# Performance work log

Measured on AMD Instinct MI355X. Metric: run time of the kernel, lower is better.

## Reference

```python
import jax, jax.numpy as jnp
import numpy as np

B, T, D, H, L = 512, 1024, 2, 32, 16  # batch, seq_len, input_dim, hidden_dim, latent_dim


def lstm_layer(x, W_ih, W_hh, b_ih, b_hh):
    """Single torch-semantics LSTM layer. x: [B, T, D_in] -> (h_seq [B,T,H], c_final [B,H]).
    Gate order matches torch: i, f, g, o."""
    Bb = x.shape[0]
    Hh = W_hh.shape[1]
    # Precompute input projection for all timesteps (one big GEMM).
    xW = jnp.einsum('btd,gd->btg', x, W_ih) + (b_ih + b_hh)  # [B, T, 4H]

    def step(carry, xw_t):
        h, c = carry
        gates = xw_t + h @ W_hh.T  # [B, 4H]
        i, f, g, o = jnp.split(gates, 4, axis=-1)
        i = jax.nn.sigmoid(i)
        f = jax.nn.sigmoid(f)
        g = jnp.tanh(g)
        o = jax.nn.sigmoid(o)
        c = f * c + i * g
        h = o * jnp.tanh(c)
        return (h, c), h

    h0 = jnp.zeros((Bb, Hh), x.dtype)
    c0 = jnp.zeros((Bb, Hh), x.dtype)
    (_, cT), h_seq = jax.lax.scan(step, (h0, c0), jnp.swapaxes(xW, 0, 1))
    return jnp.swapaxes(h_seq, 0, 1), cT


def setup_inputs() -> dict:
    key = jax.random.key(0)
    ks = jax.random.split(key, 20)
    s = 1.0 / np.sqrt(H)  # torch LSTM/Linear init scale
    u = lambda k, shape: jax.random.uniform(k, shape, jnp.float32, -s, s)
    inp = {"x": jax.random.normal(ks[0], (B, T, D), jnp.float32)}
    dims_in = [D, H, H]
    for l in range(3):
        inp[f"W_ih{l}"] = u(ks[1 + 4 * l], (4 * H, dims_in[l]))
        inp[f"W_hh{l}"] = u(ks[2 + 4 * l], (4 * H, H))
        inp[f"b_ih{l}"] = u(ks[3 + 4 * l], (4 * H,))
        inp[f"b_hh{l}"] = u(ks[4 + 4 * l], (4 * H,))
    inp["W_mean"] = u(ks[13], (L, H))
    inp["b_mean"] = u(ks[14], (L,))
    inp["W_logvar"] = u(ks[15], (L, H))
    inp["b_logvar"] = u(ks[16], (L,))
    return inp


def reference(x, W_ih0, W_hh0, b_ih0, b_hh0, W_ih1, W_hh1, b_ih1, b_hh1,
              W_ih2, W_hh2, b_ih2, b_hh2, W_mean, b_mean, W_logvar, b_logvar):
    # 3-layer LSTM (dropout inactive at inference); only top-layer final cell is used.
    h, _ = lstm_layer(x, W_ih0, W_hh0, b_ih0, b_hh0)
    h, _ = lstm_layer(h, W_ih1, W_hh1, b_ih1, b_hh1)
    _, c3 = lstm_layer(h, W_ih2, W_hh2, b_ih2, b_hh2)  # c3: [B, H]
    mean = c3 @ W_mean.T + b_mean        # [B, L]
    log_var = c3 @ W_logvar.T + b_logvar  # [B, L]
    return (mean, log_var)
```

## Files before the change

kernel.cpp:

```cpp
#include <hip/hip_runtime.h>

#define T_LEN 1024
#define HID   32
#define LDIM  16
#define BATCH 512
#define NB    8
#define NT    768
#define ROWB  80
#define SLOTB (8 * ROWB)
#define SLOT_ALL (4 * SLOTB)
#define NSLOT 8
#define LOG2E 1.44269504f

typedef _Float16 half8  __attribute__((ext_vector_type(8)));
typedef _Float16 half2v __attribute__((ext_vector_type(2)));
typedef float    f32x4  __attribute__((ext_vector_type(4)));
typedef unsigned u32;
typedef unsigned u32x4  __attribute__((ext_vector_type(4)));

#if defined(__has_builtin)
#if __has_builtin(__builtin_amdgcn_rcpf)
#define FAST_RCP(x) __builtin_amdgcn_rcpf(x)
#endif
#if __has_builtin(__builtin_amdgcn_exp2f)
#define FAST_EXP2(x) __builtin_amdgcn_exp2f(x)
#endif
#endif
#ifndef FAST_RCP
#define FAST_RCP(x) (1.0f / (x))
#endif
#ifndef FAST_EXP2
#define FAST_EXP2(x) __expf(0.69314718f * (x))
#endif

#define MFMA(a, b, c) __builtin_amdgcn_mfma_f32_16x16x32_f16((a), (b), (c), 0, 0, 0)

__device__ __forceinline__ void waitc(const u32* p, u32 need) {
    while (__hip_atomic_load(p, __ATOMIC_ACQUIRE, __HIP_MEMORY_SCOPE_WORKGROUP) < need)
        __builtin_amdgcn_s_sleep(1);
}

__global__ __launch_bounds__(NT, 1)
void lstm_encoder_kernel(const float* __restrict__ x,
                         const float* __restrict__ Wih0, const float* __restrict__ Whh0,
                         const float* __restrict__ bih0, const float* __restrict__ bhh0,
                         const float* __restrict__ Wih1, const float* __restrict__ Whh1,
                         const float* __restrict__ bih1, const float* __restrict__ bhh1,
                         const float* __restrict__ Wih2, const float* __restrict__ Whh2,
                         const float* __restrict__ bih2, const float* __restrict__ bhh2,
                         const float* __restrict__ Wm,  const float* __restrict__ bm,
                         const float* __restrict__ Wlv, const float* __restrict__ blv,
                         float* __restrict__ out)
{
    const int b0   = blockIdx.x * NB;
    const int tid  = threadIdx.x;
    const int lane = tid & 63;
    const int wave = tid >> 6;
    const int l    = wave >> 2;
    const int w    = wave & 3;
    const int n    = lane & 15;
    const int kc   = lane >> 4;
    const int nb   = n & 7;
    const int hi   = n >> 3;
    const int unit = 8 * w + 2 * kc + hi;

    __shared__ u32 xs[T_LEN * NB];
    __shared__ __align__(16) unsigned char ring[NSLOT * SLOT_ALL];
    __shared__ u32 cnt[48];
    __shared__ float cbuf[NB * HID];

    for (int i = tid; i < NB * T_LEN; i += NT) {
        const int nn = i >> 10, t = i & (T_LEN - 1);
        const float2 v = *(const float2*)(x + ((size_t)(b0 + nn) * T_LEN + t) * 2);
        half2v p; p[0] = (_Float16)v.x; p[1] = (_Float16)v.y;
        xs[t * NB + nn] = __builtin_bit_cast(u32, p);
    }
    for (int i = tid; i < (int)(sizeof(ring) / 4); i += NT) ((u32*)ring)[i] = 0u;
    if (tid < 48) cnt[tid] = 0u;

    const float* Wih = (l == 0) ? Wih0 : (l == 1) ? Wih1 : Wih2;
    const float* Whh = (l == 0) ? Whh0 : (l == 1) ? Whh1 : Whh2;
    const float* bih = (l == 0) ? bih0 : (l == 1) ? bih1 : bih2;
    const float* bhh = (l == 0) ? bhh0 : (l == 1) ? bhh1 : bhh2;

    half8 aprev[2], aself[2];
    f32x4 biasC[2];
#pragma unroll
    for (int tau = 0; tau < 2; ++tau) {
        const int   rho  = n & 1, uloc = n >> 1;
        const int   base = (tau == 0) ? (rho ? 32 : 0) : (rho ? 96 : 64);
        const int   R    = base + 8 * w + uloc;
        const float sc   = (tau == 1 && rho == 0) ? (2.0f * LOG2E) : LOG2E;
#pragma unroll
        for (int i2 = 0; i2 < 8; ++i2) {
            const int kk = kc * 8 + i2;
            aself[tau][i2] = (_Float16)(Whh[R * HID + kk] * sc);
            aprev[tau][i2] = (_Float16)(((l == 0) ? ((kk < 2) ? Wih[R * 2 + kk] : 0.0f)
                                                  : Wih[R * HID + kk]) * sc);
        }
#pragma unroll
        for (int r = 0; r < 4; ++r) {
            const int   rr    = r & 1, uD = 2 * kc + (r >> 1);
            const int   baseD = (tau == 0) ? (rr ? 32 : 0) : (rr ? 96 : 64);
            const int   RD    = baseD + 8 * w + uD;
            const float scD   = (tau == 1 && rr == 0) ? (2.0f * LOG2E) : LOG2E;
            biasC[tau][r] = (bih[RD] + bhh[RD]) * scD;
        }
    }

    const int off_r0 = ((l == 0) ? 3 : (l - 1)) * SLOTB + nb * ROWB + kc * 16;
    const int off_r1 = l * SLOTB + nb * ROWB + kc * 16;
    const int off_w  = l * SLOTB + nb * ROWB + unit * 2;
    const int off_x  = 3 * SLOTB + lane * ROWB;
    const bool xf    = (wave == 0) && (lane < NB);

    u32* cs = &cnt[l * 16];
    u32* cp = &cnt[((l > 0) ? (l - 1) : 0) * 16];
    u32* cn = &cnt[((l < 2) ? (l + 1) : 0) * 16];

    float cc = 0.0f;

    __syncthreads();
    if (xf) *(u32*)(ring + off_x) = xs[lane];
    __syncthreads();

    for (int tb = 0; tb < T_LEN; tb += NSLOT) {
#pragma unroll
        for (int s = 0; s < NSLOT; ++s) {
            const int t = tb + s;
            if (t > 0)                 waitc(cs, 4u * (u32)t);
            if (l > 0)                 waitc(cp, 4u * (u32)(t + 1));
            if (l < 2 && t >= NSLOT)   waitc(cn, 4u * (u32)(t - 7));

            u32 xw = 0;
            if (xf) {
                const int tn = (t + 1 < T_LEN) ? (t + 1) : (T_LEN - 1);
                xw = xs[tn * NB + lane];
            }
            const half8 bf0 = __builtin_bit_cast(half8,
                *(const u32x4*)(ring + s * SLOT_ALL + off_r0));
            const half8 bf1 = __builtin_bit_cast(half8,
                *(const u32x4*)(ring + ((s + 7) & 7) * SLOT_ALL + off_r1));

            f32x4 ac0 = MFMA(aprev[0], bf0, biasC[0]);
            f32x4 ac1 = MFMA(aprev[1], bf0, biasC[1]);
            ac0 = MFMA(aself[0], bf1, ac0);
            ac1 = MFMA(aself[1], bf1, ac1);

            const float ai  = hi ? ac0[2] : ac0[0];
            const float af_ = hi ? ac0[3] : ac0[1];
            const float ag  = hi ? ac1[2] : ac1[0];
            const float ao  = hi ? ac1[3] : ac1[1];

            const float ei = FAST_EXP2(-ai);
            const float ef = FAST_EXP2(-af_);
            const float eg = FAST_EXP2(-ag);
            const float eo = FAST_EXP2(-ao);
            const float p1  = (1.0f + ei) * (1.0f + eg);
            const float den = p1 * (1.0f + ef);
            const float tmn = (1.0f - eg) * (1.0f + ef);
            float c_ = fmaf(cc, p1, tmn) * FAST_RCP(den);
            c_ = fminf(fmaxf(c_, -20.0f), 20.0f);
            cc = c_;
            const float ec = FAST_EXP2(-2.0f * LOG2E * c_);
            const float hv = (1.0f - ec) * FAST_RCP((1.0f + eo) * (1.0f + ec));

            *(_Float16*)(ring + s * SLOT_ALL + off_w) = (_Float16)hv;
            if (xf) *(u32*)(ring + ((s + 1) & 7) * SLOT_ALL + off_x) = xw;

            if (lane == 0)
                __hip_atomic_fetch_add(cs, 1u, __ATOMIC_RELEASE,
                                       __HIP_MEMORY_SCOPE_WORKGROUP);
        }
    }

    if (l == 2) cbuf[nb * HID + unit] = cc;
    __syncthreads();

    if (tid < NB * 2 * LDIM) {
        const int  nn = tid >> 5;
        const int  o  = tid & 31;
        const bool is_mean = (o < LDIM);
        const int  jo = o & (LDIM - 1);
        const float* W  = is_mean ? Wm : Wlv;
        float acc = is_mean ? bm[jo] : blv[jo];
#pragma unroll
        for (int k = 0; k < HID; ++k) acc = fmaf(W[jo * HID + k], cbuf[nn * HID + k], acc);
        out[(is_mean ? 0 : (size_t)BATCH * LDIM) + (size_t)(b0 + nn) * LDIM + jo] = acc;
    }
}

extern "C" void kernel_launch(void* const* d_in, const int* in_sizes, int n_in,
                              void* d_out, int out_size, void* d_ws, size_t ws_size,
                              hipStream_t stream) {
    const float* x    = (const float*)d_in[0];
    const float* Wih0 = (const float*)d_in[1];
    const float* Whh0 = (const float*)d_in[2];
    const float* bih0 = (const float*)d_in[3];
    const float* bhh0 = (const float*)d_in[4];
    const float* Wih1 = (const float*)d_in[5];
    const float* Whh1 = (const float*)d_in[6];
    const float* bih1 = (const float*)d_in[7];
    const float* bhh1 = (const float*)d_in[8];
    const float* Wih2 = (const float*)d_in[9];
    const float* Whh2 = (const float*)d_in[10];
    const float* bih2 = (const float*)d_in[11];
    const float* bhh2 = (const float*)d_in[12];
    const float* Wm   = (const float*)d_in[13];
    const float* bm   = (const float*)d_in[14];
    const float* Wlv  = (const float*)d_in[15];
    const float* blv  = (const float*)d_in[16];
    float* out = (float*)d_out;

    lstm_encoder_kernel<<<dim3(BATCH / NB), dim3(NT), 0, stream>>>(
        x, Wih0, Whh0, bih0, bhh0, Wih1, Whh1, bih1, bhh1,
        Wih2, Whh2, bih2, bhh2, Wm, bm, Wlv, blv, out);
}
```

Before: 437.9 us.

## Halve batch per block to 4, 2 waves per layer with 4 MFMAs each

Drops the batch per block from 8 to 4 and the threads from 768 to 384, so each layer runs on 2 waves instead of 4. Each wave now issues 4 MFMAs per input, sharing one B fragment across 16 hidden units. Layer 0 no longer runs an input MFMA; it adds the 2-wide input projection with scalar FMAs from the xs array, which also removes the x-slot ring traffic. The change also reorders waves across layers, raises wave priority around the critical compute, and lengthens the spin sleep. Twice as many blocks (128) gives more CU parallelism, at the cost of a longer serial chain of MFMAs per wave per timestep.

```diff
diff --git a/kernel.cpp b/kernel.cpp
--- a/kernel.cpp
+++ b/kernel.cpp
@@ -4,11 +4,8 @@
 #define HID   32
 #define LDIM  16
 #define BATCH 512
-#define NB    8
-#define NT    768
-#define ROWB  80
-#define SLOTB (8 * ROWB)
-#define SLOT_ALL (4 * SLOTB)
+#define NB    4
+#define NT    384
 #define NSLOT 8
 #define LOG2E 1.44269504f
 
@@ -37,7 +34,7 @@
 
 __device__ __forceinline__ void waitc(const u32* p, u32 need) {
     while (__hip_atomic_load(p, __ATOMIC_ACQUIRE, __HIP_MEMORY_SCOPE_WORKGROUP) < need)
-        __builtin_amdgcn_s_sleep(1);
+        __builtin_amdgcn_s_sleep(2);
 }
 
 __global__ __launch_bounds__(NT, 1)
@@ -56,23 +53,23 @@
     const int tid  = threadIdx.x;
     const int lane = tid & 63;
     const int wave = tid >> 6;
-    const int l    = wave >> 2;
-    const int w    = wave & 3;
+    const int l    = (wave < 2) ? 1 : (wave < 4) ? 0 : 2;
+    const int v    = wave & 1;
     const int n    = lane & 15;
     const int kc   = lane >> 4;
-    const int nb   = n & 7;
-    const int hi   = n >> 3;
-    const int unit = 8 * w + 2 * kc + hi;
+    const int nb   = n & 3;
+    const int hi   = n >> 2;
+    const int unit = 16 * v + 4 * hi + kc;
 
     __shared__ u32 xs[T_LEN * NB];
-    __shared__ __align__(16) unsigned char ring[NSLOT * SLOT_ALL];
+    __shared__ __align__(16) u32x4 ring[3][NSLOT][4][NB];
     __shared__ u32 cnt[48];
     __shared__ float cbuf[NB * HID];
 
     for (int i = tid; i < NB * T_LEN; i += NT) {
         const int nn = i >> 10, t = i & (T_LEN - 1);
-        const float2 v = *(const float2*)(x + ((size_t)(b0 + nn) * T_LEN + t) * 2);
-        half2v p; p[0] = (_Float16)v.x; p[1] = (_Float16)v.y;
+        const float2 vv = *(const float2*)(x + ((size_t)(b0 + nn) * T_LEN + t) * 2);
+        half2v p; p[0] = (_Float16)vv.x; p[1] = (_Float16)vv.y;
         xs[t * NB + nn] = __builtin_bit_cast(u32, p);
     }
     for (int i = tid; i < (int)(sizeof(ring) / 4); i += NT) ((u32*)ring)[i] = 0u;
@@ -83,36 +80,33 @@
     const float* bih = (l == 0) ? bih0 : (l == 1) ? bih1 : bih2;
     const float* bhh = (l == 0) ? bhh0 : (l == 1) ? bhh1 : bhh2;
 
-    half8 aprev[2], aself[2];
-    f32x4 biasC[2];
-#pragma unroll
-    for (int tau = 0; tau < 2; ++tau) {
-        const int   rho  = n & 1, uloc = n >> 1;
-        const int   base = (tau == 0) ? (rho ? 32 : 0) : (rho ? 96 : 64);
-        const int   R    = base + 8 * w + uloc;
-        const float sc   = (tau == 1 && rho == 0) ? (2.0f * LOG2E) : LOG2E;
-#pragma unroll
-        for (int i2 = 0; i2 < 8; ++i2) {
-            const int kk = kc * 8 + i2;
-            aself[tau][i2] = (_Float16)(Whh[R * HID + kk] * sc);
-            aprev[tau][i2] = (_Float16)(((l == 0) ? ((kk < 2) ? Wih[R * 2 + kk] : 0.0f)
-                                                  : Wih[R * HID + kk]) * sc);
+    half8 aprev[4], aself[4];
+    f32x4 biasC[4];
+    float wx0v[4], wx1v[4];
+#pragma unroll
+    for (int tau = 0; tau < 4; ++tau) {
+        const int   R  = (n & 3) * 32 + 16 * v + 4 * tau + (n >> 2);
+        const float sc = ((n & 3) == 2) ? (2.0f * LOG2E) : LOG2E;
+#pragma unroll
+        for (int e = 0; e < 8; ++e) {
+            const int kk = 8 * kc + e;
+            aself[tau][e] = (_Float16)(Whh[R * HID + kk] * sc);
+            aprev[tau][e] = (l > 0) ? (_Float16)(Wih[R * HID + kk] * sc) : (_Float16)0.0f;
         }
 #pragma unroll
         for (int r = 0; r < 4; ++r) {
-            const int   rr    = r & 1, uD = 2 * kc + (r >> 1);
-            const int   baseD = (tau == 0) ? (rr ? 32 : 0) : (rr ? 96 : 64);
-            const int   RD    = baseD + 8 * w + uD;
-            const float scD   = (tau == 1 && rr == 0) ? (2.0f * LOG2E) : LOG2E;
+            const int   RD  = r * 32 + 16 * v + 4 * tau + kc;
+            const float scD = (r == 2) ? (2.0f * LOG2E) : LOG2E;
             biasC[tau][r] = (bih[RD] + bhh[RD]) * scD;
         }
     }
-
-    const int off_r0 = ((l == 0) ? 3 : (l - 1)) * SLOTB + nb * ROWB + kc * 16;
-    const int off_r1 = l * SLOTB + nb * ROWB + kc * 16;
-    const int off_w  = l * SLOTB + nb * ROWB + unit * 2;
-    const int off_x  = 3 * SLOTB + lane * ROWB;
-    const bool xf    = (wave == 0) && (lane < NB);
+#pragma unroll
+    for (int r = 0; r < 4; ++r) {
+        const int   RD  = r * 32 + unit;
+        const float scD = (r == 2) ? (2.0f * LOG2E) : LOG2E;
+        wx0v[r] = (l == 0) ? Wih[RD * 2 + 0] * scD : 0.0f;
+        wx1v[r] = (l == 0) ? Wih[RD * 2 + 1] * scD : 0.0f;
+    }
 
     u32* cs = &cnt[l * 16];
     u32* cp = &cnt[((l > 0) ? (l - 1) : 0) * 16];
@@ -121,41 +115,52 @@
     float cc = 0.0f;
 
     __syncthreads();
-    if (xf) *(u32*)(ring + off_x) = xs[lane];
-    __syncthreads();
 
     for (int tb = 0; tb < T_LEN; tb += NSLOT) {
 #pragma unroll
         for (int s = 0; s < NSLOT; ++s) {
             const int t = tb + s;
-            if (t > 0)                 waitc(cs, 4u * (u32)t);
-            if (l > 0)                 waitc(cp, 4u * (u32)(t + 1));
-            if (l < 2 && t >= NSLOT)   waitc(cn, 4u * (u32)(t - 7));
-
-            u32 xw = 0;
-            if (xf) {
-                const int tn = (t + 1 < T_LEN) ? (t + 1) : (T_LEN - 1);
-                xw = xs[tn * NB + lane];
+            if (t > 0)               waitc(cs, 2u * (u32)t);
+            if (l > 0)               waitc(cp, 2u * (u32)(t + 1));
+            if (l < 2 && t >= NSLOT) waitc(cn, 2u * (u32)(t - (NSLOT - 1)));
+
+            const u32x4 bf1 = ring[l][(s + NSLOT - 1) & (NSLOT - 1)][kc][nb];
+
+            __builtin_amdgcn_s_setprio(1);
+            f32x4 a0, a1, a2, a3;
+            if (l == 0) {
+                a0 = MFMA(aself[0], __builtin_bit_cast(half8, bf1), biasC[0]);
+                a1 = MFMA(aself[1], __builtin_bit_cast(half8, bf1), biasC[1]);
+                a2 = MFMA(aself[2], __builtin_bit_cast(half8, bf1), biasC[2]);
+                a3 = MFMA(aself[3], __builtin_bit_cast(half8, bf1), biasC[3]);
+            } else {
+                const u32x4 bf0 = ring[l - 1][s][kc][nb];
+                a0 = MFMA(aprev[0], __builtin_bit_cast(half8, bf0), biasC[0]);
+                a1 = MFMA(aprev[1], __builtin_bit_cast(half8, bf0), biasC[1]);
+                a2 = MFMA(aprev[2], __builtin_bit_cast(half8, bf0), biasC[2]);
+                a3 = MFMA(aprev[3], __builtin_bit_cast(half8, bf0), biasC[3]);
+                a0 = MFMA(aself[0], __builtin_bit_cast(half8, bf1), a0);
+                a1 = MFMA(aself[1], __builtin_bit_cast(half8, bf1), a1);
+                a2 = MFMA(aself[2], __builtin_bit_cast(half8, bf1), a2);
+                a3 = MFMA(aself[3], __builtin_bit_cast(half8, bf1), a3);
             }
-            const half8 bf0 = __builtin_bit_cast(half8,
-                *(const u32x4*)(ring + s * SLOT_ALL + off_r0));
-            const half8 bf1 = __builtin_bit_cast(half8,
-                *(const u32x4*)(ring + ((s + 7) & 7) * SLOT_ALL + off_r1));
-
-            f32x4 ac0 = MFMA(aprev[0], bf0, biasC[0]);
-            f32x4 ac1 = MFMA(aprev[1], bf0, biasC[1]);
-            ac0 = MFMA(aself[0], bf1, ac0);
-            ac1 = MFMA(aself[1], bf1, ac1);
-
-            const float ai  = hi ? ac0[2] : ac0[0];
-            const float af_ = hi ? ac0[3] : ac0[1];
-            const float ag  = hi ? ac1[2] : ac1[0];
-            const float ao  = hi ? ac1[3] : ac1[1];
-
-            const float ei = FAST_EXP2(-ai);
-            const float ef = FAST_EXP2(-af_);
-            const float eg = FAST_EXP2(-ag);
-            const float eo = FAST_EXP2(-ao);
+
+#define SELR(r) ((hi & 2) ? ((hi & 1) ? a3[r] : a2[r]) : ((hi & 1) ? a1[r] : a0[r]))
+            float gi = SELR(0), gf = SELR(1), gg = SELR(2), go = SELR(3);
+#undef SELR
+            if (l == 0) {
+                const half2v xp = __builtin_bit_cast(half2v, xs[t * NB + nb]);
+                const float x0 = (float)xp[0], x1 = (float)xp[1];
+                gi = fmaf(wx1v[0], x1, fmaf(wx0v[0], x0, gi));
+                gf = fmaf(wx1v[1], x1, fmaf(wx0v[1], x0, gf));
+                gg = fmaf(wx1v[2], x1, fmaf(wx0v[2], x0, gg));
+                go = fmaf(wx1v[3], x1, fmaf(wx0v[3], x0, go));
+            }
+
+            const float ei  = FAST_EXP2(-gi);
+            const float ef  = FAST_EXP2(-gf);
+            const float eg  = FAST_EXP2(-gg);
+            const float eo  = FAST_EXP2(-go);
             const float p1  = (1.0f + ei) * (1.0f + eg);
             const float den = p1 * (1.0f + ef);
             const float tmn = (1.0f - eg) * (1.0f + ef);
@@ -165,12 +170,11 @@
             const float ec = FAST_EXP2(-2.0f * LOG2E * c_);
             const float hv = (1.0f - ec) * FAST_RCP((1.0f + eo) * (1.0f + ec));
 
-            *(_Float16*)(ring + s * SLOT_ALL + off_w) = (_Float16)hv;
-            if (xf) *(u32*)(ring + ((s + 1) & 7) * SLOT_ALL + off_x) = xw;
+            *(_Float16*)((char*)&ring[l][s][unit >> 3][nb] + (unit & 7) * 2) = (_Float16)hv;
+            __builtin_amdgcn_s_setprio(0);
 
             if (lane == 0)
-                __hip_atomic_fetch_add(cs, 1u, __ATOMIC_RELEASE,
-                                       __HIP_MEMORY_SCOPE_WORKGROUP);
+                __hip_atomic_fetch_add(cs, 1u, __ATOMIC_RELEASE, __HIP_MEMORY_SCOPE_WORKGROUP);
         }
     }
 
```

Measured after the change: 482.0 us. 1.1x slower.
